# Performance work log

Measured on AMD Instinct MI355X. Metric: run time of the kernel, lower is better.

## Reference

```python
import jax, jax.numpy as jnp
import numpy as np

BS, C, H, W = 8, 256, 64, 64
INNER = 256

def setup_inputs() -> dict:
    key = jax.random.key(0)
    ks = jax.random.split(key, 9)
    s = 0.02
    return {
        "x": jax.random.normal(ks[0], (BS, C, H, W), jnp.float32),
        "Wq": jax.random.normal(ks[1], (INNER, C), jnp.float32) * s,
        "bq": jax.random.normal(ks[2], (INNER,), jnp.float32) * s,
        "Wk": jax.random.normal(ks[3], (INNER, C), jnp.float32) * s,
        "bk": jax.random.normal(ks[4], (INNER,), jnp.float32) * s,
        "Wv": jax.random.normal(ks[5], (INNER, C), jnp.float32) * s,
        "bv": jax.random.normal(ks[6], (INNER,), jnp.float32) * s,
        "Wo": jax.random.normal(ks[7], (C, INNER), jnp.float32) * s,
        "bo": jax.random.normal(ks[8], (C,), jnp.float32) * s,
    }

def reference(x, Wq, bq, Wk, bk, Wv, bv, Wo, bo):
    bs, c, h, w = x.shape
    L = h * w
    # (bs, C, H, W) -> (bs, L, C)
    t = x.reshape(bs, c, L).transpose(0, 2, 1)
    q = t @ Wq.T + bq   # (bs, L, inner)
    k = t @ Wk.T + bk
    v = t @ Wv.T + bv
    # torch code divides by np.round(np.sqrt(inner_dim), 2)
    scale = np.round(np.sqrt(q.shape[-1]), 2).astype(np.float32)
    scores = jnp.einsum('bld,bmd->blm', q, k) / scale   # (bs, L, L)
    factors = jax.nn.softmax(scores, axis=-1)
    ctx = jnp.einsum('blm,bmd->bld', factors, v)        # (bs, L, inner)
    out = ctx @ Wo.T + bo                               # (bs, L, C)
    return out.transpose(0, 2, 1).reshape(bs, c, h, w)
```

## Files before the change

kernel.cpp:

```cpp
#include <hip/hip_runtime.h>
#include <stdint.h>

#define BS   8
#define CH   256
#define LSEQ 4096
#define DIN  256
#define NT2  128
#define KT2  32

typedef __bf16 bf16x8 __attribute__((ext_vector_type(8)));
typedef __bf16 bf16x4 __attribute__((ext_vector_type(4)));
typedef float  f32x4  __attribute__((ext_vector_type(4)));

__device__ __forceinline__ void gload_lds16(const void* g, void* l) {
    __builtin_amdgcn_global_load_lds(
        (const __attribute__((address_space(1))) uint32_t*)g,
        (__attribute__((address_space(3))) uint32_t*)l, 16, 0, 0);
}

#define CEXP_FOLD (1.4426950408889634f / 16.0f)

__global__ __launch_bounds__(256) void qkv_proj_kernel(
    const float* __restrict__ x,
    const float* __restrict__ Wq, const float* __restrict__ bq,
    const float* __restrict__ Wk, const float* __restrict__ bk,
    const float* __restrict__ Wv, const float* __restrict__ bv,
    __bf16* __restrict__ Q, uint8_t* __restrict__ KV)
{
    const int b     = blockIdx.z;
    const int which = blockIdx.y;
    const int l0    = blockIdx.x * 64;

    const float* W    = (which == 0) ? Wq : (which == 1) ? Wk : Wv;
    const float* bias = (which == 0) ? bq : (which == 1) ? bk : bv;
    const float* X    = x + (size_t)b * CH * LSEQ;

    __shared__ __align__(16) __bf16 sXt[64][40];
    __shared__ __align__(16) __bf16 sW[256][40];

    const int tid  = threadIdx.x;
    const int wv   = tid >> 6;
    const int lane = tid & 63;
    const int g    = lane >> 4;
    const int n16  = lane & 15;

    f32x4 acc[4][4];
    #pragma unroll
    for (int i = 0; i < 4; ++i)
        #pragma unroll
        for (int j = 0; j < 4; ++j)
            acc[i][j] = f32x4{0.f, 0.f, 0.f, 0.f};

    for (int kk = 0; kk < 8; ++kk) {
        const int c0 = kk * 32;
        __syncthreads();
        #pragma unroll
        for (int p = 0; p < 8; ++p) {
            const int i  = p * 32 + (tid >> 3);
            const int c4 = (tid & 7) * 4;
            const float4 v = *(const float4*)(W + (size_t)i * CH + c0 + c4);
            bf16x4 pk = { (__bf16)v.x, (__bf16)v.y, (__bf16)v.z, (__bf16)v.w };
            *(bf16x4*)&sW[i][c4] = pk;
        }
        #pragma unroll
        for (int p = 0; p < 2; ++p) {
            const int c  = p * 16 + (tid >> 4);
            const int l4 = (tid & 15) * 4;
            const float4 v = *(const float4*)(X + (size_t)(c0 + c) * LSEQ + l0 + l4);
            sXt[l4 + 0][c] = (__bf16)v.x;
            sXt[l4 + 1][c] = (__bf16)v.y;
            sXt[l4 + 2][c] = (__bf16)v.z;
            sXt[l4 + 3][c] = (__bf16)v.w;
        }
        __syncthreads();

        bf16x8 af[4], bfr[4];
        #pragma unroll
        for (int mr = 0; mr < 4; ++mr)
            af[mr] = *(const bf16x8*)&sXt[mr * 16 + n16][g * 8];
        #pragma unroll
        for (int nc = 0; nc < 4; ++nc)
            bfr[nc] = *(const bf16x8*)&sW[wv * 64 + nc * 16 + n16][g * 8];
        #pragma unroll
        for (int mr = 0; mr < 4; ++mr)
            #pragma unroll
            for (int nc = 0; nc < 4; ++nc)
                acc[mr][nc] = __builtin_amdgcn_mfma_f32_16x16x32_bf16(
                    af[mr], bfr[nc], acc[mr][nc], 0, 0, 0);
    }

    if (which == 0) {
        __bf16* out = Q + (size_t)b * LSEQ * DIN;
        #pragma unroll
        for (int nc = 0; nc < 4; ++nc) {
            const int icol = wv * 64 + nc * 16 + n16;
            const float bb = bias[icol];
            #pragma unroll
            for (int mr = 0; mr < 4; ++mr) {
                const int lrow = l0 + mr * 16 + g * 4;
                #pragma unroll
                for (int r = 0; r < 4; ++r)
                    out[(size_t)(lrow + r) * DIN + icol] =
                        (__bf16)((acc[mr][nc][r] + bb) * CEXP_FOLD);
            }
        }
    } else if (which == 1) {
        #pragma unroll
        for (int nc = 0; nc < 4; ++nc) {
            const int icol = wv * 64 + nc * 16 + n16;
            const float bb = bias[icol];
            #pragma unroll
            for (int mr = 0; mr < 4; ++mr) {
                #pragma unroll
                for (int r = 0; r < 4; ++r) {
                    const int lrow = l0 + mr * 16 + g * 4 + r;
                    const int t2 = lrow >> 5, row = lrow & 31;
                    const size_t off = ((size_t)(b * NT2 + t2) << 15)
                                     + (size_t)row * 512
                                     + ((icol * 2) ^ ((row & 7) << 4));
                    *(__bf16*)(KV + off) = (__bf16)(acc[mr][nc][r] + bb);
                }
            }
        }
    } else {
        #pragma unroll
        for (int nc = 0; nc < 4; ++nc) {
            const int d  = wv * 64 + nc * 16 + n16;
            const float bb = bias[d];
            #pragma unroll
            for (int mr = 0; mr < 4; ++mr) {
                const int lrow = l0 + mr * 16 + g * 4;
                const int t2 = lrow >> 5, c = lrow & 31;
                bf16x4 pk;
                #pragma unroll
                for (int r = 0; r < 4; ++r)
                    pk[r] = (__bf16)(acc[mr][nc][r] + bb);
                const size_t off = ((size_t)(b * NT2 + t2) << 15) + 16384
                                 + (size_t)(d >> 1) * 128
                                 + ((((d & 1) * 64) + 2 * c) ^ (((d >> 1) & 7) << 4));
                *(bf16x4*)(KV + off) = pk;
            }
        }
    }
}

__global__ __launch_bounds__(256) void attn_kernel(
    const __bf16* __restrict__ Q, const uint8_t* __restrict__ KV,
    __bf16* __restrict__ O)
{
    const int b   = blockIdx.x;
    const int q0  = blockIdx.y * 64;
    const int tid = threadIdx.x;
    const int wv  = tid >> 6, lane = tid & 63, g = lane >> 4, n16 = lane & 15;

    __shared__ __align__(1024) uint8_t sKV[2][32768];
    __shared__ __align__(1024) uint8_t sP[4096];

    bf16x8 qf[8];
    {
        const __bf16* Qrow = Q + ((size_t)b * LSEQ + q0 + wv * 16 + n16) * DIN;
        #pragma unroll
        for (int ks = 0; ks < 8; ++ks)
            qf[ks] = *(const bf16x8*)(Qrow + ks * 32 + g * 8);
    }

    bf16x8 onesf;
    #pragma unroll
    for (int j = 0; j < 8; ++j) onesf[j] = (__bf16)1.0f;

    float m_i = -__builtin_inff();
    f32x4 accO[16];
    #pragma unroll
    for (int ds = 0; ds < 16; ++ds) accO[ds] = f32x4{0.f, 0.f, 0.f, 0.f};
    f32x4 accL = f32x4{0.f, 0.f, 0.f, 0.f};

    const uint8_t* KVb = KV + ((size_t)b * NT2 << 15);
    const float DEFER_TH = 8.0f;

    #pragma unroll
    for (int p = 0; p < 8; ++p) {
        const int off = p * 4096 + tid * 16;
        gload_lds16(KVb + off, &sKV[0][off]);
    }

    const int prow  = wv * 16 + n16;
    const int pbase = (prow >> 1) * 128;
    const int pswz  = ((prow >> 1) & 7) << 4;
    const int phalf = (prow & 1) * 64;

    for (int t = 0; t < NT2; ++t) {
        const int buf = t & 1;
        if (t + 1 < NT2) {
            const uint8_t* src = KVb + ((size_t)(t + 1) << 15);
            #pragma unroll
            for (int p = 0; p < 8; ++p) {
                const int off = p * 4096 + tid * 16;
                gload_lds16(src + off, &sKV[buf ^ 1][off]);
            }
            asm volatile("s_waitcnt vmcnt(8)" ::: "memory");
        } else {
            asm volatile("s_waitcnt vmcnt(0)" ::: "memory");
        }
        __builtin_amdgcn_s_barrier();
        asm volatile("" ::: "memory");

        const uint8_t* kb = sKV[buf];

        f32x4 st0 = f32x4{0.f, 0.f, 0.f, 0.f};
        f32x4 st1 = f32x4{0.f, 0.f, 0.f, 0.f};
        __builtin_amdgcn_s_setprio(1);
        #pragma unroll
        for (int ks = 0; ks < 8; ++ks) {
            const int r0 = n16;
            const int r1 = 16 + n16;
            const bf16x8 kf0 = *(const bf16x8*)(kb + r0 * 512
                                + ((ks * 64 + g * 16) ^ ((r0 & 7) << 4)));
            const bf16x8 kf1 = *(const bf16x8*)(kb + r1 * 512
                                + ((ks * 64 + g * 16) ^ ((r1 & 7) << 4)));
            st0 = __builtin_amdgcn_mfma_f32_16x16x32_bf16(kf0, qf[ks], st0, 0, 0, 0);
            st1 = __builtin_amdgcn_mfma_f32_16x16x32_bf16(kf1, qf[ks], st1, 0, 0, 0);
        }
        __builtin_amdgcn_s_setprio(0);

        float mx = fmaxf(fmaxf(fmaxf(st0[0], st0[1]), fmaxf(st0[2], st0[3])),
                         fmaxf(fmaxf(st1[0], st1[1]), fmaxf(st1[2], st1[3])));
        mx = fmaxf(mx, __shfl_xor(mx, 16));
        mx = fmaxf(mx, __shfl_xor(mx, 32));
        if (!__all(mx - m_i <= DEFER_TH)) {
            const float mnew = fmaxf(m_i, mx);
            const float scl  = exp2f(m_i - mnew);
            m_i = mnew;
            float sclr[4];
            #pragma unroll
            for (int r = 0; r < 4; ++r)
                sclr[r] = __shfl(scl, g * 4 + r);
            #pragma unroll
            for (int ds = 0; ds < 16; ++ds)
                #pragma unroll
                for (int r = 0; r < 4; ++r)
                    accO[ds][r] *= sclr[r];
            #pragma unroll
            for (int r = 0; r < 4; ++r)
                accL[r] *= sclr[r];
        }

        {
            bf16x4 pk0, pk1;
            #pragma unroll
            for (int r = 0; r < 4; ++r) {
                pk0[r] = (__bf16)exp2f(st0[r] - m_i);
                pk1[r] = (__bf16)exp2f(st1[r] - m_i);
            }
            const int c0b = 2 * (g * 4);
            *(bf16x4*)(sP + pbase + ((phalf + c0b) ^ pswz))      = pk0;
            *(bf16x4*)(sP + pbase + ((phalf + c0b + 32) ^ pswz)) = pk1;
        }

        bf16x8 af;
        {
            const int row = wv * 16 + n16;
            af = *(const bf16x8*)(sP + (row >> 1) * 128
                   + ((((row & 1) * 64) + g * 16) ^ (((row >> 1) & 7) << 4)));
        }
        __builtin_amdgcn_s_setprio(1);
        #pragma unroll
        for (int ds = 0; ds < 16; ++ds) {
            const int d = ds * 16 + n16;
            const bf16x8 vf = *(const bf16x8*)(kb + 16384 + (d >> 1) * 128
                               + ((((d & 1) * 64) + g * 16) ^ (((d >> 1) & 7) << 4)));
            accO[ds] = __builtin_amdgcn_mfma_f32_16x16x32_bf16(af, vf, accO[ds], 0, 0, 0);
        }
        accL = __builtin_amdgcn_mfma_f32_16x16x32_bf16(af, onesf, accL, 0, 0, 0);
        __builtin_amdgcn_s_setprio(0);

        asm volatile("" ::: "memory");
        __builtin_amdgcn_s_barrier();
    }

    float inv[4];
    #pragma unroll
    for (int r = 0; r < 4; ++r) inv[r] = 1.f / accL[r];
    __bf16* Ob = O + ((size_t)b * LSEQ + q0 + wv * 16) * DIN;
    #pragma unroll
    for (int ds = 0; ds < 16; ++ds)
        #pragma unroll
        for (int r = 0; r < 4; ++r)
            Ob[(size_t)(g * 4 + r) * DIN + ds * 16 + n16] = (__bf16)(accO[ds][r] * inv[r]);
}

__global__ __launch_bounds__(256) void out_proj_kernel(
    const float* __restrict__ Wo, const float* __restrict__ bo,
    const __bf16* __restrict__ O, float* __restrict__ out)
{
    const int b   = blockIdx.z;
    const int c0  = blockIdx.y * 64;
    const int l0  = blockIdx.x * 256;
    const int tid = threadIdx.x;
    const int wv  = tid >> 6, lane = tid & 63, g = lane >> 4, n16 = lane & 15;

    __shared__ __align__(16) __bf16 sWo[64][40];
    __shared__ __align__(16) __bf16 sO[256][40];

    const __bf16* Ob = O + (size_t)b * LSEQ * DIN;

    f32x4 acc[4][4];
    #pragma unroll
    for (int i = 0; i < 4; ++i)
        #pragma unroll
        for (int j = 0; j < 4; ++j)
            acc[i][j] = f32x4{0.f, 0.f, 0.f, 0.f};

    for (int kk = 0; kk < 8; ++kk) {
        const int i0 = kk * 32;
        __syncthreads();
        #pragma unroll
        for (int p = 0; p < 2; ++p) {
            const int c  = p * 32 + (tid >> 3);
            const int i4 = (tid & 7) * 4;
            const float4 v = *(const float4*)(Wo + (size_t)(c0 + c) * DIN + i0 + i4);
            bf16x4 pk = { (__bf16)v.x, (__bf16)v.y, (__bf16)v.z, (__bf16)v.w };
            *(bf16x4*)&sWo[c][i4] = pk;
        }
        #pragma unroll
        for (int p = 0; p < 4; ++p) {
            const int l  = p * 64 + (tid >> 2);
            const int sg = tid & 3;
            *(uint4*)&sO[l][sg * 8] = *(const uint4*)(Ob + (size_t)(l0 + l) * DIN + i0 + sg * 8);
        }
        __syncthreads();

        bf16x8 af[4], bfr[4];
        #pragma unroll
        for (int mr = 0; mr < 4; ++mr)
            af[mr] = *(const bf16x8*)&sWo[mr * 16 + n16][g * 8];
        #pragma unroll
        for (int nc = 0; nc < 4; ++nc)
            bfr[nc] = *(const bf16x8*)&sO[wv * 64 + nc * 16 + n16][g * 8];
        #pragma unroll
        for (int mr = 0; mr < 4; ++mr)
            #pragma unroll
            for (int nc = 0; nc < 4; ++nc)
                acc[mr][nc] = __builtin_amdgcn_mfma_f32_16x16x32_bf16(
                    af[mr], bfr[nc], acc[mr][nc], 0, 0, 0);
    }

    #pragma unroll
    for (int mr = 0; mr < 4; ++mr) {
        const int c = c0 + mr * 16 + g * 4;
        #pragma unroll
        for (int nc = 0; nc < 4; ++nc) {
            const int l = l0 + wv * 64 + nc * 16 + n16;
            #pragma unroll
            for (int r = 0; r < 4; ++r)
                out[((size_t)b * CH + c + r) * LSEQ + l] = acc[mr][nc][r] + bo[c + r];
        }
    }
}

extern "C" void kernel_launch(void* const* d_in, const int* in_sizes, int n_in,
                              void* d_out, int out_size, void* d_ws, size_t ws_size,
                              hipStream_t stream)
{
    const float* x  = (const float*)d_in[0];
    const float* Wq = (const float*)d_in[1];
    const float* bq = (const float*)d_in[2];
    const float* Wk = (const float*)d_in[3];
    const float* bk = (const float*)d_in[4];
    const float* Wv = (const float*)d_in[5];
    const float* bv = (const float*)d_in[6];
    const float* Wo = (const float*)d_in[7];
    const float* bo = (const float*)d_in[8];
    float* out = (float*)d_out;

    __bf16*  Q  = (__bf16*)d_ws;
    uint8_t* KV = (uint8_t*)d_ws + (16u << 20);
    __bf16*  O  = (__bf16*)((uint8_t*)d_ws + (48u << 20));

    qkv_proj_kernel<<<dim3(LSEQ / 64, 3, BS), 256, 0, stream>>>(
        x, Wq, bq, Wk, bk, Wv, bv, Q, KV);
    attn_kernel<<<dim3(BS, LSEQ / 64), 256, 0, stream>>>(Q, KV, O);
    out_proj_kernel<<<dim3(LSEQ / 256, CH / 64, BS), 256, 0, stream>>>(Wo, bo, O, out);
}
```

Measured before the change: 262.6 us.

## Use 32x32 MFMA for PV with shared rescale, fuse QKV projections per tile

The attention PV product now uses 32x32x16 MFMA tiles, with each wave covering 32 query rows by 128 output dims instead of 16 rows by all 256 dims. Row scale factors move through shared memory with an extra __syncthreads per tile, and the row sum is kept as a scalar from exp values rather than through a ones-vector MFMA. The QKV projection kernel loads and converts the x tile once, then loops over Q, K and V instead of launching a separate block for each. This removes repeated x loads and the extra row-sum MFMA, at the cost of an added block barrier per KV tile and fewer, longer projection blocks.

```diff
diff --git a/kernel.cpp b/kernel.cpp
--- a/kernel.cpp
+++ b/kernel.cpp
@@ -11,6 +11,7 @@
 typedef __bf16 bf16x8 __attribute__((ext_vector_type(8)));
 typedef __bf16 bf16x4 __attribute__((ext_vector_type(4)));
 typedef float  f32x4  __attribute__((ext_vector_type(4)));
+typedef float  f32x16 __attribute__((ext_vector_type(16)));
 
 __device__ __forceinline__ void gload_lds16(const void* g, void* l) {
     __builtin_amdgcn_global_load_lds(
@@ -27,15 +28,11 @@
     const float* __restrict__ Wv, const float* __restrict__ bv,
     __bf16* __restrict__ Q, uint8_t* __restrict__ KV)
 {
-    const int b     = blockIdx.z;
-    const int which = blockIdx.y;
-    const int l0    = blockIdx.x * 64;
-
-    const float* W    = (which == 0) ? Wq : (which == 1) ? Wk : Wv;
-    const float* bias = (which == 0) ? bq : (which == 1) ? bk : bv;
-    const float* X    = x + (size_t)b * CH * LSEQ;
-
-    __shared__ __align__(16) __bf16 sXt[64][40];
+    const int b  = blockIdx.y;
+    const int l0 = blockIdx.x * 64;
+    const float* X = x + (size_t)b * CH * LSEQ;
+
+    __shared__ __align__(16) __bf16 sXt[64][264];
     __shared__ __align__(16) __bf16 sW[256][40];
 
     const int tid  = threadIdx.x;
@@ -44,101 +41,107 @@
     const int g    = lane >> 4;
     const int n16  = lane & 15;
 
-    f32x4 acc[4][4];
-    #pragma unroll
-    for (int i = 0; i < 4; ++i)
-        #pragma unroll
-        for (int j = 0; j < 4; ++j)
-            acc[i][j] = f32x4{0.f, 0.f, 0.f, 0.f};
-
-    for (int kk = 0; kk < 8; ++kk) {
-        const int c0 = kk * 32;
-        __syncthreads();
-        #pragma unroll
-        for (int p = 0; p < 8; ++p) {
-            const int i  = p * 32 + (tid >> 3);
-            const int c4 = (tid & 7) * 4;
-            const float4 v = *(const float4*)(W + (size_t)i * CH + c0 + c4);
-            bf16x4 pk = { (__bf16)v.x, (__bf16)v.y, (__bf16)v.z, (__bf16)v.w };
-            *(bf16x4*)&sW[i][c4] = pk;
-        }
-        #pragma unroll
-        for (int p = 0; p < 2; ++p) {
-            const int c  = p * 16 + (tid >> 4);
-            const int l4 = (tid & 15) * 4;
-            const float4 v = *(const float4*)(X + (size_t)(c0 + c) * LSEQ + l0 + l4);
-            sXt[l4 + 0][c] = (__bf16)v.x;
-            sXt[l4 + 1][c] = (__bf16)v.y;
-            sXt[l4 + 2][c] = (__bf16)v.z;
-            sXt[l4 + 3][c] = (__bf16)v.w;
-        }
-        __syncthreads();
-
-        bf16x8 af[4], bfr[4];
-        #pragma unroll
-        for (int mr = 0; mr < 4; ++mr)
-            af[mr] = *(const bf16x8*)&sXt[mr * 16 + n16][g * 8];
-        #pragma unroll
-        for (int nc = 0; nc < 4; ++nc)
-            bfr[nc] = *(const bf16x8*)&sW[wv * 64 + nc * 16 + n16][g * 8];
-        #pragma unroll
-        for (int mr = 0; mr < 4; ++mr)
+    #pragma unroll
+    for (int p = 0; p < 16; ++p) {
+        const int c  = p * 16 + (tid >> 4);
+        const int l4 = (tid & 15) * 4;
+        const float4 v = *(const float4*)(X + (size_t)c * LSEQ + l0 + l4);
+        sXt[l4 + 0][c] = (__bf16)v.x;
+        sXt[l4 + 1][c] = (__bf16)v.y;
+        sXt[l4 + 2][c] = (__bf16)v.z;
+        sXt[l4 + 3][c] = (__bf16)v.w;
+    }
+
+    for (int which = 0; which < 3; ++which) {
+        const float* W    = (which == 0) ? Wq : (which == 1) ? Wk : Wv;
+        const float* bias = (which == 0) ? bq : (which == 1) ? bk : bv;
+
+        f32x4 acc[4][4];
+        #pragma unroll
+        for (int i = 0; i < 4; ++i)
+            #pragma unroll
+            for (int j = 0; j < 4; ++j)
+                acc[i][j] = f32x4{0.f, 0.f, 0.f, 0.f};
+
+        for (int kk = 0; kk < 8; ++kk) {
+            const int c0 = kk * 32;
+            __syncthreads();
+            #pragma unroll
+            for (int p = 0; p < 8; ++p) {
+                const int i  = p * 32 + (tid >> 3);
+                const int c4 = (tid & 7) * 4;
+                const float4 v = *(const float4*)(W + (size_t)i * CH + c0 + c4);
+                bf16x4 pk = { (__bf16)v.x, (__bf16)v.y, (__bf16)v.z, (__bf16)v.w };
+                *(bf16x4*)&sW[i][c4] = pk;
+            }
+            __syncthreads();
+
+            bf16x8 af[4], bfr[4];
+            #pragma unroll
+            for (int mr = 0; mr < 4; ++mr)
+                af[mr] = *(const bf16x8*)&sXt[mr * 16 + n16][c0 + g * 8];
             #pragma unroll
             for (int nc = 0; nc < 4; ++nc)
-                acc[mr][nc] = __builtin_amdgcn_mfma_f32_16x16x32_bf16(
-                    af[mr], bfr[nc], acc[mr][nc], 0, 0, 0);
-    }
-
-    if (which == 0) {
-        __bf16* out = Q + (size_t)b * LSEQ * DIN;
-        #pragma unroll
-        for (int nc = 0; nc < 4; ++nc) {
-            const int icol = wv * 64 + nc * 16 + n16;
-            const float bb = bias[icol];
-            #pragma unroll
-            for (int mr = 0; mr < 4; ++mr) {
-                const int lrow = l0 + mr * 16 + g * 4;
+                bfr[nc] = *(const bf16x8*)&sW[wv * 64 + nc * 16 + n16][g * 8];
+            #pragma unroll
+            for (int mr = 0; mr < 4; ++mr)
                 #pragma unroll
-                for (int r = 0; r < 4; ++r)
-                    out[(size_t)(lrow + r) * DIN + icol] =
-                        (__bf16)((acc[mr][nc][r] + bb) * CEXP_FOLD);
-            }
-        }
-    } else if (which == 1) {
-        #pragma unroll
-        for (int nc = 0; nc < 4; ++nc) {
-            const int icol = wv * 64 + nc * 16 + n16;
-            const float bb = bias[icol];
-            #pragma unroll
-            for (int mr = 0; mr < 4; ++mr) {
+                for (int nc = 0; nc < 4; ++nc)
+                    acc[mr][nc] = __builtin_amdgcn_mfma_f32_16x16x32_bf16(
+                        af[mr], bfr[nc], acc[mr][nc], 0, 0, 0);
+        }
+
+        if (which == 0) {
+            __bf16* out = Q + (size_t)b * LSEQ * DIN;
+            #pragma unroll
+            for (int nc = 0; nc < 4; ++nc) {
+                const int icol = wv * 64 + nc * 16 + n16;
+                const float bb = bias[icol];
                 #pragma unroll
-                for (int r = 0; r < 4; ++r) {
-                    const int lrow = l0 + mr * 16 + g * 4 + r;
-                    const int t2 = lrow >> 5, row = lrow & 31;
-                    const size_t off = ((size_t)(b * NT2 + t2) << 15)
-                                     + (size_t)row * 512
-                                     + ((icol * 2) ^ ((row & 7) << 4));
-                    *(__bf16*)(KV + off) = (__bf16)(acc[mr][nc][r] + bb);
+                for (int mr = 0; mr < 4; ++mr) {
+                    const int lrow = l0 + mr * 16 + g * 4;
+                    #pragma unroll
+                    for (int r = 0; r < 4; ++r)
+                        out[(size_t)(lrow + r) * DIN + icol] =
+                            (__bf16)((acc[mr][nc][r] + bb) * CEXP_FOLD);
                 }
             }
-        }
-    } else {
-        #pragma unroll
-        for (int nc = 0; nc < 4; ++nc) {
-            const int d  = wv * 64 + nc * 16 + n16;
-            const float bb = bias[d];
-            #pragma unroll
-            for (int mr = 0; mr < 4; ++mr) {
-                const int lrow = l0 + mr * 16 + g * 4;
-                const int t2 = lrow >> 5, c = lrow & 31;
-                bf16x4 pk;
+        } else if (which == 1) {
+            #pragma unroll
+            for (int nc = 0; nc < 4; ++nc) {
+                const int icol = wv * 64 + nc * 16 + n16;
+                const float bb = bias[icol];
                 #pragma unroll
-                for (int r = 0; r < 4; ++r)
-                    pk[r] = (__bf16)(acc[mr][nc][r] + bb);
-                const size_t off = ((size_t)(b * NT2 + t2) << 15) + 16384
-                                 + (size_t)(d >> 1) * 128
-                                 + ((((d & 1) * 64) + 2 * c) ^ (((d >> 1) & 7) << 4));
-                *(bf16x4*)(KV + off) = pk;
+                for (int mr = 0; mr < 4; ++mr) {
+                    #pragma unroll
+                    for (int r = 0; r < 4; ++r) {
+                        const int lrow = l0 + mr * 16 + g * 4 + r;
+                        const int t2 = lrow >> 5, row = lrow & 31;
+                        const size_t off = ((size_t)(b * NT2 + t2) << 15)
+                                         + (size_t)row * 512
+                                         + ((icol * 2) ^ ((row & 7) << 4));
+                        *(__bf16*)(KV + off) = (__bf16)(acc[mr][nc][r] + bb);
+                    }
+                }
+            }
+        } else {
+            #pragma unroll
+            for (int nc = 0; nc < 4; ++nc) {
+                const int d  = wv * 64 + nc * 16 + n16;
+                const float bb = bias[d];
+                #pragma unroll
+                for (int mr = 0; mr < 4; ++mr) {
+                    const int lrow = l0 + mr * 16 + g * 4;
+                    const int t2 = lrow >> 5, c = lrow & 31;
+                    bf16x4 pk;
+                    #pragma unroll
+                    for (int r = 0; r < 4; ++r)
+                        pk[r] = (__bf16)(acc[mr][nc][r] + bb);
+                    const size_t off = ((size_t)(b * NT2 + t2) << 15) + 16384
+                                     + (size_t)(d >> 1) * 128
+                                     + ((((d & 1) * 64) + 2 * c) ^ (((d >> 1) & 7) << 4));
+                    *(bf16x4*)(KV + off) = pk;
+                }
             }
         }
     }
@@ -152,9 +155,14 @@
     const int q0  = blockIdx.y * 64;
     const int tid = threadIdx.x;
     const int wv  = tid >> 6, lane = tid & 63, g = lane >> 4, n16 = lane & 15;
+    const int l31 = lane & 31, l5 = lane >> 5;
+    const int qh  = wv >> 1, dh = wv & 1;
 
     __shared__ __align__(1024) uint8_t sKV[2][32768];
     __shared__ __align__(1024) uint8_t sP[4096];
+    __shared__ float    shS[64];
+    __shared__ float    shL[64];
+    __shared__ uint32_t shFlg[4];
 
     bf16x8 qf[8];
     {
@@ -164,15 +172,14 @@
             qf[ks] = *(const bf16x8*)(Qrow + ks * 32 + g * 8);
     }
 
-    bf16x8 onesf;
-    #pragma unroll
-    for (int j = 0; j < 8; ++j) onesf[j] = (__bf16)1.0f;
-
     float m_i = -__builtin_inff();
-    f32x4 accO[16];
-    #pragma unroll
-    for (int ds = 0; ds < 16; ++ds) accO[ds] = f32x4{0.f, 0.f, 0.f, 0.f};
-    f32x4 accL = f32x4{0.f, 0.f, 0.f, 0.f};
+    float l_i = 0.f;
+    f32x16 accO[4];
+    #pragma unroll
+    for (int dgi = 0; dgi < 4; ++dgi)
+        #pragma unroll
+        for (int j = 0; j < 16; ++j)
+            accO[dgi][j] = 0.f;
 
     const uint8_t* KVb = KV + ((size_t)b * NT2 << 15);
     const float DEFER_TH = 8.0f;
@@ -226,66 +233,89 @@
                          fmaxf(fmaxf(st1[0], st1[1]), fmaxf(st1[2], st1[3])));
         mx = fmaxf(mx, __shfl_xor(mx, 16));
         mx = fmaxf(mx, __shfl_xor(mx, 32));
+        float scl = 1.f;
+        uint32_t resc = 0;
         if (!__all(mx - m_i <= DEFER_TH)) {
             const float mnew = fmaxf(m_i, mx);
-            const float scl  = exp2f(m_i - mnew);
+            scl = exp2f(m_i - mnew);
             m_i = mnew;
-            float sclr[4];
-            #pragma unroll
-            for (int r = 0; r < 4; ++r)
-                sclr[r] = __shfl(scl, g * 4 + r);
-            #pragma unroll
-            for (int ds = 0; ds < 16; ++ds)
-                #pragma unroll
-                for (int r = 0; r < 4; ++r)
-                    accO[ds][r] *= sclr[r];
-            #pragma unroll
-            for (int r = 0; r < 4; ++r)
-                accL[r] *= sclr[r];
+            l_i *= scl;
+            resc = 1;
         }
 
         {
+            float pv0[4], pv1[4];
             bf16x4 pk0, pk1;
             #pragma unroll
             for (int r = 0; r < 4; ++r) {
-                pk0[r] = (__bf16)exp2f(st0[r] - m_i);
-                pk1[r] = (__bf16)exp2f(st1[r] - m_i);
-            }
+                pv0[r] = exp2f(st0[r] - m_i);
+                pv1[r] = exp2f(st1[r] - m_i);
+                pk0[r] = (__bf16)pv0[r];
+                pk1[r] = (__bf16)pv1[r];
+            }
+            float s = ((pv0[0] + pv0[1]) + (pv0[2] + pv0[3]))
+                    + ((pv1[0] + pv1[1]) + (pv1[2] + pv1[3]));
+            s += __shfl_xor(s, 16);
+            s += __shfl_xor(s, 32);
+            l_i += s;
             const int c0b = 2 * (g * 4);
             *(bf16x4*)(sP + pbase + ((phalf + c0b) ^ pswz))      = pk0;
             *(bf16x4*)(sP + pbase + ((phalf + c0b + 32) ^ pswz)) = pk1;
         }
-
-        bf16x8 af;
-        {
-            const int row = wv * 16 + n16;
-            af = *(const bf16x8*)(sP + (row >> 1) * 128
-                   + ((((row & 1) * 64) + g * 16) ^ (((row >> 1) & 7) << 4)));
-        }
+        if (lane < 16) shS[wv * 16 + lane] = scl;
+        if (lane == 0) shFlg[wv] = resc;
+        __syncthreads();
+
+        const uint32_t any = shFlg[0] | shFlg[1] | shFlg[2] | shFlg[3];
+        if (any) {
+            float sr[16];
+            #pragma unroll
+            for (int j = 0; j < 16; ++j)
+                sr[j] = shS[qh * 32 + (j & 3) + 8 * (j >> 2) + 4 * l5];
+            #pragma unroll
+            for (int dgi = 0; dgi < 4; ++dgi)
+                #pragma unroll
+                for (int j = 0; j < 16; ++j)
+                    accO[dgi][j] *= sr[j];
+        }
+
         __builtin_amdgcn_s_setprio(1);
         #pragma unroll
-        for (int ds = 0; ds < 16; ++ds) {
-            const int d = ds * 16 + n16;
-            const bf16x8 vf = *(const bf16x8*)(kb + 16384 + (d >> 1) * 128
-                               + ((((d & 1) * 64) + g * 16) ^ (((d >> 1) & 7) << 4)));
-            accO[ds] = __builtin_amdgcn_mfma_f32_16x16x32_bf16(af, vf, accO[ds], 0, 0, 0);
-        }
-        accL = __builtin_amdgcn_mfma_f32_16x16x32_bf16(af, onesf, accL, 0, 0, 0);
+        for (int kh = 0; kh < 2; ++kh) {
+            const int arow = qh * 32 + l31;
+            const int boff = 32 * kh + 16 * l5;
+            const bf16x8 af = *(const bf16x8*)(sP + (arow >> 1) * 128
+                               + ((((arow & 1) * 64) + boff) ^ (((arow >> 1) & 7) << 4)));
+            #pragma unroll
+            for (int dgi = 0; dgi < 4; ++dgi) {
+                const int d = dh * 128 + dgi * 32 + l31;
+                const bf16x8 vf = *(const bf16x8*)(kb + 16384 + (d >> 1) * 128
+                                   + ((((d & 1) * 64) + boff) ^ (((d >> 1) & 7) << 4)));
+                accO[dgi] = __builtin_amdgcn_mfma_f32_32x32x16_bf16(af, vf, accO[dgi], 0, 0, 0);
+            }
+        }
         __builtin_amdgcn_s_setprio(0);
 
         asm volatile("" ::: "memory");
         __builtin_amdgcn_s_barrier();
     }
 
-    float inv[4];
-    #pragma unroll
-    for (int r = 0; r < 4; ++r) inv[r] = 1.f / accL[r];
-    __bf16* Ob = O + ((size_t)b * LSEQ + q0 + wv * 16) * DIN;
-    #pragma unroll
-    for (int ds = 0; ds < 16; ++ds)
-        #pragma unroll
-        for (int r = 0; r < 4; ++r)
-            Ob[(size_t)(g * 4 + r) * DIN + ds * 16 + n16] = (__bf16)(accO[ds][r] * inv[r]);
+    if (lane < 16) shL[wv * 16 + lane] = l_i;
+    __syncthreads();
+    float inv[16];
+    #pragma unroll
+    for (int j = 0; j < 16; ++j)
+        inv[j] = 1.f / shL[qh * 32 + (j & 3) + 8 * (j >> 2) + 4 * l5];
+    __bf16* Ob = O + ((size_t)b * LSEQ + q0 + qh * 32) * DIN;
+    #pragma unroll
+    for (int dgi = 0; dgi < 4; ++dgi) {
+        #pragma unroll
+        for (int j = 0; j < 16; ++j) {
+            const int row = (j & 3) + 8 * (j >> 2) + 4 * l5;
+            Ob[(size_t)row * DIN + dh * 128 + dgi * 32 + l31] =
+                (__bf16)(accO[dgi][j] * inv[j]);
+        }
+    }
 }
 
 __global__ __launch_bounds__(256) void out_proj_kernel(
@@ -376,7 +406,7 @@
     uint8_t* KV = (uint8_t*)d_ws + (16u << 20);
     __bf16*  O  = (__bf16*)((uint8_t*)d_ws + (48u << 20));
 
-    qkv_proj_kernel<<<dim3(LSEQ / 64, 3, BS), 256, 0, stream>>>(
+    qkv_proj_kernel<<<dim3(LSEQ / 64, BS), 256, 0, stream>>>(
         x, Wq, bq, Wk, bk, Wv, bv, Q, KV);
     attn_kernel<<<dim3(BS, LSEQ / 64), 256, 0, stream>>>(Q, KV, O);
     out_proj_kernel<<<dim3(LSEQ / 256, CH / 64, BS), 256, 0, stream>>>(Wo, bo, O, out);
```

Result: slower. 293.3 us (+11.7%).

## Split PV output across waves by head dim and share P tile via LDS

Applied to the files above, without the earlier changes.

The PV matmul is repartitioned so each wave owns a 64-column slice of the head dimension for all 64 query rows, instead of all 256 columns for its own 16 rows. Each V fragment loaded from LDS is now reused across four query groups, cutting V LDS reads per wave to a quarter. The row sum is computed with shuffles in fp32 rather than with a ones-vector MFMA. The cost is an extra block barrier per tile to publish P, the rescale factors and the rescale flags, and any wave's rescale now forces every wave to rescale.

```diff
diff --git a/kernel.cpp b/kernel.cpp
--- a/kernel.cpp
+++ b/kernel.cpp
@@ -155,6 +155,9 @@
 
     __shared__ __align__(1024) uint8_t sKV[2][32768];
     __shared__ __align__(1024) uint8_t sP[4096];
+    __shared__ float    shS[64];
+    __shared__ float    shL[64];
+    __shared__ uint32_t shFlg[4];
 
     bf16x8 qf[8];
     {
@@ -164,15 +167,14 @@
             qf[ks] = *(const bf16x8*)(Qrow + ks * 32 + g * 8);
     }
 
-    bf16x8 onesf;
-    #pragma unroll
-    for (int j = 0; j < 8; ++j) onesf[j] = (__bf16)1.0f;
-
     float m_i = -__builtin_inff();
-    f32x4 accO[16];
-    #pragma unroll
-    for (int ds = 0; ds < 16; ++ds) accO[ds] = f32x4{0.f, 0.f, 0.f, 0.f};
-    f32x4 accL = f32x4{0.f, 0.f, 0.f, 0.f};
+    float l_i = 0.f;
+    f32x4 accO[4][4];
+    #pragma unroll
+    for (int qg = 0; qg < 4; ++qg)
+        #pragma unroll
+        for (int dg = 0; dg < 4; ++dg)
+            accO[qg][dg] = f32x4{0.f, 0.f, 0.f, 0.f};
 
     const uint8_t* KVb = KV + ((size_t)b * NT2 << 15);
     const float DEFER_TH = 8.0f;
@@ -226,66 +228,99 @@
                          fmaxf(fmaxf(st1[0], st1[1]), fmaxf(st1[2], st1[3])));
         mx = fmaxf(mx, __shfl_xor(mx, 16));
         mx = fmaxf(mx, __shfl_xor(mx, 32));
+        float scl = 1.f;
+        uint32_t resc = 0;
         if (!__all(mx - m_i <= DEFER_TH)) {
             const float mnew = fmaxf(m_i, mx);
-            const float scl  = exp2f(m_i - mnew);
+            scl = exp2f(m_i - mnew);
             m_i = mnew;
-            float sclr[4];
-            #pragma unroll
-            for (int r = 0; r < 4; ++r)
-                sclr[r] = __shfl(scl, g * 4 + r);
-            #pragma unroll
-            for (int ds = 0; ds < 16; ++ds)
-                #pragma unroll
-                for (int r = 0; r < 4; ++r)
-                    accO[ds][r] *= sclr[r];
-            #pragma unroll
-            for (int r = 0; r < 4; ++r)
-                accL[r] *= sclr[r];
+            l_i *= scl;
+            resc = 1;
         }
 
         {
+            float pv0[4], pv1[4];
             bf16x4 pk0, pk1;
             #pragma unroll
             for (int r = 0; r < 4; ++r) {
-                pk0[r] = (__bf16)exp2f(st0[r] - m_i);
-                pk1[r] = (__bf16)exp2f(st1[r] - m_i);
-            }
+                pv0[r] = exp2f(st0[r] - m_i);
+                pv1[r] = exp2f(st1[r] - m_i);
+                pk0[r] = (__bf16)pv0[r];
+                pk1[r] = (__bf16)pv1[r];
+            }
+            float s = ((pv0[0] + pv0[1]) + (pv0[2] + pv0[3]))
+                    + ((pv1[0] + pv1[1]) + (pv1[2] + pv1[3]));
+            s += __shfl_xor(s, 16);
+            s += __shfl_xor(s, 32);
+            l_i += s;
             const int c0b = 2 * (g * 4);
             *(bf16x4*)(sP + pbase + ((phalf + c0b) ^ pswz))      = pk0;
             *(bf16x4*)(sP + pbase + ((phalf + c0b + 32) ^ pswz)) = pk1;
         }
-
-        bf16x8 af;
-        {
-            const int row = wv * 16 + n16;
-            af = *(const bf16x8*)(sP + (row >> 1) * 128
-                   + ((((row & 1) * 64) + g * 16) ^ (((row >> 1) & 7) << 4)));
+        if (lane < 16) shS[wv * 16 + lane] = scl;
+        if (lane == 0) shFlg[wv] = resc;
+        asm volatile("s_waitcnt lgkmcnt(0)" ::: "memory");
+        __builtin_amdgcn_s_barrier();
+        asm volatile("" ::: "memory");
+
+        const uint32_t any = shFlg[0] | shFlg[1] | shFlg[2] | shFlg[3];
+        if (any) {
+            #pragma unroll
+            for (int qg = 0; qg < 4; ++qg) {
+                float sr[4];
+                #pragma unroll
+                for (int r = 0; r < 4; ++r)
+                    sr[r] = shS[qg * 16 + g * 4 + r];
+                #pragma unroll
+                for (int dg = 0; dg < 4; ++dg)
+                    #pragma unroll
+                    for (int r = 0; r < 4; ++r)
+                        accO[qg][dg][r] *= sr[r];
+            }
+        }
+
+        bf16x8 af[4];
+        #pragma unroll
+        for (int qg = 0; qg < 4; ++qg) {
+            const int arow = qg * 16 + n16;
+            af[qg] = *(const bf16x8*)(sP + (arow >> 1) * 128
+                       + ((((arow & 1) * 64) + g * 16) ^ (((arow >> 1) & 7) << 4)));
         }
         __builtin_amdgcn_s_setprio(1);
         #pragma unroll
-        for (int ds = 0; ds < 16; ++ds) {
-            const int d = ds * 16 + n16;
+        for (int dg = 0; dg < 4; ++dg) {
+            const int d = wv * 64 + dg * 16 + n16;
             const bf16x8 vf = *(const bf16x8*)(kb + 16384 + (d >> 1) * 128
                                + ((((d & 1) * 64) + g * 16) ^ (((d >> 1) & 7) << 4)));
-            accO[ds] = __builtin_amdgcn_mfma_f32_16x16x32_bf16(af, vf, accO[ds], 0, 0, 0);
-        }
-        accL = __builtin_amdgcn_mfma_f32_16x16x32_bf16(af, onesf, accL, 0, 0, 0);
+            #pragma unroll
+            for (int qg = 0; qg < 4; ++qg)
+                accO[qg][dg] = __builtin_amdgcn_mfma_f32_16x16x32_bf16(
+                    af[qg], vf, accO[qg][dg], 0, 0, 0);
+        }
         __builtin_amdgcn_s_setprio(0);
 
         asm volatile("" ::: "memory");
         __builtin_amdgcn_s_barrier();
     }
 
-    float inv[4];
-    #pragma unroll
-    for (int r = 0; r < 4; ++r) inv[r] = 1.f / accL[r];
-    __bf16* Ob = O + ((size_t)b * LSEQ + q0 + wv * 16) * DIN;
-    #pragma unroll
-    for (int ds = 0; ds < 16; ++ds)
+    if (lane < 16) shL[wv * 16 + lane] = l_i;
+    __syncthreads();
+    __bf16* Ob = O + ((size_t)b * LSEQ + q0) * DIN;
+    #pragma unroll
+    for (int qg = 0; qg < 4; ++qg) {
+        float inv[4];
         #pragma unroll
         for (int r = 0; r < 4; ++r)
-            Ob[(size_t)(g * 4 + r) * DIN + ds * 16 + n16] = (__bf16)(accO[ds][r] * inv[r]);
+            inv[r] = 1.f / shL[qg * 16 + g * 4 + r];
+        #pragma unroll
+        for (int dg = 0; dg < 4; ++dg) {
+            const int dcol = wv * 64 + dg * 16 + n16;
+            #pragma unroll
+            for (int r = 0; r < 4; ++r)
+                Ob[(size_t)(qg * 16 + g * 4 + r) * DIN + dcol] =
+                    (__bf16)(accO[qg][dg][r] * inv[r]);
+        }
+    }
 }
 
 __global__ __launch_bounds__(256) void out_proj_kernel(
```

Measured after the change: 264.8 us. No clear change (+0.8%).
